# Kernel tuning notes

Hardware: AMD Instinct MI355X
Metric: run time of the kernel (lower is better)

## Reference

```python
import jax, jax.numpy as jnp
import numpy as np

KSIZE = 7       # patch size
STRIDE_Q = 4    # stride_1: query patch stride
STRIDE_KV = 1   # stride_2: key/value patch stride
SCALE = 10.0    # softmax_scale


def unfold(x, k, stride, pad):
    """torch.nn.Unfold equivalent. x:[B,C,H,W] -> [B, C*k*k, L] (c-major, then kh, kw)."""
    x = jnp.pad(x, ((0, 0), (0, 0), (pad, pad), (pad, pad)))
    B, C, Hp, Wp = x.shape
    nh = (Hp - k) // stride + 1
    nw = (Wp - k) // stride + 1
    sl = lambda i, n: slice(i, i + (n - 1) * stride + 1, stride)
    # [B, C, k*k, nh, nw]
    pat = jnp.stack([x[:, :, sl(i, nh), sl(j, nw)] for i in range(k) for j in range(k)], axis=2)
    return pat.reshape(B, C * k * k, nh * nw)


def fold(p, k, stride, pad, H, W):
    """torch.nn.functional.fold equivalent (overlap-add). p:[B, C*k*k, L] -> [B,C,H,W]."""
    B, D, L = p.shape
    C = D // (k * k)
    nh = (H + 2 * pad - k) // stride + 1
    nw = (W + 2 * pad - k) // stride + 1
    p = p.reshape(B, C, k, k, nh, nw)
    out = jnp.zeros((B, C, H + 2 * pad, W + 2 * pad), p.dtype)
    sl = lambda i, n: slice(i, i + (n - 1) * stride + 1, stride)
    for i in range(k):
        for j in range(k):
            out = out.at[:, :, sl(i, nh), sl(j, nw)].add(p[:, :, i, j])
    return out[:, :, pad:pad + H, pad:pad + W]


def conv1x1(x, w, bias):
    # w: [out, in]
    return jnp.einsum('bihw,oi->bohw', x, w) + bias[None, :, None, None]


def setup_inputs() -> dict:
    key = jax.random.key(0)
    ks = jax.random.split(key, 9)
    B, Cin, H, W = 4, 64, 128, 128
    Cit = 16
    s_in = 1.0 / np.sqrt(Cin)
    s_it = 1.0 / np.sqrt(Cit)
    return {
        'b': jax.random.normal(ks[0], (B, Cin, H, W), jnp.float32),
        'g_w': jax.random.normal(ks[1], (Cit, Cin), jnp.float32) * s_in,
        'g_b': jax.random.normal(ks[2], (Cit,), jnp.float32) * 0.01,
        'th_w': jax.random.normal(ks[3], (Cit, Cin), jnp.float32) * s_in,
        'th_b': jax.random.normal(ks[4], (Cit,), jnp.float32) * 0.01,
        'ph_w': jax.random.normal(ks[5], (Cit, Cin), jnp.float32) * s_in,
        'ph_b': jax.random.normal(ks[6], (Cit,), jnp.float32) * 0.01,
        'o_w': jax.random.normal(ks[7], (Cin, Cit), jnp.float32) * s_it,
        'o_b': jax.random.normal(ks[8], (Cin,), jnp.float32) * 0.01,
    }


def reference(b, g_w, g_b, th_w, th_b, ph_w, ph_b, o_w, o_b):
    B, Cin, H, W = b.shape
    pad = KSIZE // 2
    b1 = conv1x1(b, g_w, g_b)      # queries source  [B,16,H,W]
    b2 = conv1x1(b, th_w, th_b)    # values source
    b3 = conv1x1(b, ph_w, ph_b)    # keys source

    Q = unfold(b1, KSIZE, STRIDE_Q, pad).transpose(0, 2, 1)   # [B, L1, D]
    K = unfold(b3, KSIZE, STRIDE_KV, pad).transpose(0, 2, 1)  # [B, L2, D]
    V = unfold(b2, KSIZE, STRIDE_KV, pad).transpose(0, 2, 1)  # [B, L2, D]

    scores = jnp.einsum('bqd,bkd->bqk', Q, K)                 # [B, L1, L2]
    attn = jax.nn.softmax(scores * SCALE, axis=-1)
    Zp = jnp.einsum('bqk,bkd->bqd', attn, V).transpose(0, 2, 1)  # [B, D, L1]

    y = fold(Zp, KSIZE, STRIDE_Q, pad, H, W)                  # overlap-add
    Zc = fold(jnp.ones_like(Zp), KSIZE, STRIDE_Q, pad, H, W)  # overlap counts
    y = y / Zc
    y = conv1x1(y, o_w, o_b)
    return b + y
```

## Files before the change

### kernel.cpp

```cpp
#include <hip/hip_runtime.h>
#include <math.h>

#define NB 4
#define CIN 64
#define CIT 16
#define KS 7
#define PAD 3
#define HH 128
#define WW 128
#define HP 134
#define WPS 136
#define L1 1024
#define DD 784
#define SCALE_F 10.0f
#define WSCR 4.0f
#define TCAP 128

#define NPIX (HP * WPS)
#define NHWCF (NB * NPIX * CIT)
#define RSTR 2176

typedef __attribute__((ext_vector_type(4))) float f32x4;
typedef __attribute__((ext_vector_type(8))) short s16x8;
typedef __attribute__((ext_vector_type(4))) unsigned int u32x4;

__device__ __forceinline__ unsigned short f2bf(float f) {
    unsigned u = __float_as_uint(f);
    unsigned r = (u + 0x7FFFu + ((u >> 16) & 1u)) >> 16;
    return (unsigned short)r;
}

__global__ __launch_bounds__(256) void k_prep(
    const float* __restrict__ bin,
    const float* __restrict__ gw, const float* __restrict__ gb,
    const float* __restrict__ tw, const float* __restrict__ tb,
    const float* __restrict__ pw, const float* __restrict__ pb,
    float* __restrict__ b1f, float* __restrict__ b2f, float* __restrict__ b3f,
    unsigned short* __restrict__ b1n, unsigned short* __restrict__ b3n)
{
    int p = blockIdx.x * 256 + threadIdx.x;
    if (p >= NB * NPIX) return;
    int x = p % WPS; int r = p / WPS; int y = r % HP; int bb = r / HP;
    bool inter = (x >= PAD && x < PAD + WW && y >= PAD && y < PAD + HH);
    float v[CIN];
    if (inter) {
        int iy = y - PAD, ix = x - PAD;
        const float* src = bin + ((size_t)(bb * CIN) * HH + iy) * WW + ix;
        #pragma unroll
        for (int ci = 0; ci < CIN; ++ci) v[ci] = src[ci * HH * WW];
    }
    float a1v[CIT], a2v[CIT], a3v[CIT];
    unsigned short o1[CIT], o3[CIT];
    #pragma unroll
    for (int co = 0; co < CIT; ++co) {
        float a1 = 0.f, a2 = 0.f, a3 = 0.f;
        if (inter) {
            a1 = gb[co]; a2 = tb[co]; a3 = pb[co];
            #pragma unroll
            for (int ci = 0; ci < CIN; ++ci) {
                float vv = v[ci];
                a1 += gw[co * CIN + ci] * vv;
                a2 += tw[co * CIN + ci] * vv;
                a3 += pw[co * CIN + ci] * vv;
            }
        }
        a1v[co] = a1; a2v[co] = a2; a3v[co] = a3;
        o1[co] = f2bf(a1); o3[co] = f2bf(a3);
    }
    size_t pb16 = (size_t)p * CIT;
    #pragma unroll
    for (int g = 0; g < 4; ++g) {
        f32x4 w1 = {a1v[4*g], a1v[4*g+1], a1v[4*g+2], a1v[4*g+3]};
        f32x4 w2 = {a2v[4*g], a2v[4*g+1], a2v[4*g+2], a2v[4*g+3]};
        f32x4 w3 = {a3v[4*g], a3v[4*g+1], a3v[4*g+2], a3v[4*g+3]};
        *(f32x4*)(b1f + pb16 + 4*g) = w1;
        *(f32x4*)(b2f + pb16 + 4*g) = w2;
        *(f32x4*)(b3f + pb16 + 4*g) = w3;
    }
    unsigned pk1[8], pk3[8];
    #pragma unroll
    for (int kk = 0; kk < 8; ++kk) {
        pk1[kk] = (unsigned)o1[2 * kk] | ((unsigned)o1[2 * kk + 1] << 16);
        pk3[kk] = (unsigned)o3[2 * kk] | ((unsigned)o3[2 * kk + 1] << 16);
    }
    unsigned short* d1 = b1n + pb16;
    unsigned short* d3 = b3n + pb16;
    u32x4 w1a = {pk1[0], pk1[1], pk1[2], pk1[3]}, w1b = {pk1[4], pk1[5], pk1[6], pk1[7]};
    u32x4 w3a = {pk3[0], pk3[1], pk3[2], pk3[3]}, w3b = {pk3[4], pk3[5], pk3[6], pk3[7]};
    *(u32x4*)d1 = w1a; *(u32x4*)(d1 + 8) = w1b;
    *(u32x4*)d3 = w3a; *(u32x4*)(d3 + 8) = w3b;
}

__global__ __launch_bounds__(512, 2) void k_screen(
    const unsigned short* __restrict__ b1n, const unsigned short* __restrict__ b3n,
    _Float16* __restrict__ tmaxh)
{
    int blk = blockIdx.x;
    int qt = blk & 3;
    int qh = (blk >> 2) & 31;
    int bb = blk >> 7;
    int qstart_ky = qt * 32;
    int tid = threadIdx.x;
    int lane = tid & 63, w = tid >> 6;
    int lanelow = lane & 15;
    int h = (lane >> 5) & 1;
    int clo = (lane >> 4) & 1;

    __shared__ __align__(16) short smem[16 * RSTR];

    const unsigned short* b1nb = b1n + (size_t)bb * (NPIX * CIT);
    const unsigned short* b3nb = b3n + (size_t)bb * (NPIX * CIT);

    int qybase = 4 * qh;
    size_t qb0 = ((size_t)((bb * 64 + 2 * qh) * 16 + lanelow)) * 1024 + qt * 256 + w;
    size_t qb1 = ((size_t)((bb * 64 + 2 * qh + 1) * 16 + lanelow)) * 1024 + qt * 256 + w;

    for (int task = tid; task < 1600; task += 512) {
        int pp = task % 50, qq = task / 50;
        u32x4 lo = {0, 0, 0, 0}, hi = {0, 0, 0, 0};
        if (pp < 49) {
            int i = pp / 7, j = pp % 7;
            int qx = 4 * qq;
            const unsigned short* src = b1nb + ((size_t)(qybase + i) * WPS + qx + j) * CIT;
            lo = *(const u32x4*)src; hi = *(const u32x4*)(src + 8);
        }
        short* dst = smem + (qq * 50 + pp) * 16;
        *(u32x4*)dst = lo; *(u32x4*)(dst + 8) = hi;
    }
    __syncthreads();

    s16x8 B0[25], B1[25];
    #pragma unroll
    for (int s = 0; s < 25; ++s) {
        int ko = s * 32 + ((lane >> 4) & 3) * 8;
        B0[s] = *(const s16x8*)(smem + lanelow * 800 + ko);
        B1[s] = *(const s16x8*)(smem + (lanelow + 16) * 800 + ko);
    }
    __syncthreads();

    short* kring = smem;
    for (int task = tid; task < 16 * 272; task += 512) {
        int rr = task / 272, ch = task % 272;
        *(u32x4*)(kring + rr * RSTR + ch * 8) =
            *(const u32x4*)(b3nb + (size_t)(qstart_ky + rr) * (WPS * CIT) + ch * 8);
    }
    __syncthreads();

    int abase = (w * 16 + lanelow) * 16 + clo * 8;

    for (int p = 0; p < 4; ++p) {
        __builtin_amdgcn_s_setprio(1);
        for (int it8 = 0; it8 < 8; ++it8) {
            int it = 8 * p + it8;
            int ky = qstart_ky + it;
            f32x4 C0 = {0.f, 0.f, 0.f, 0.f}, C1 = {0.f, 0.f, 0.f, 0.f};
            #pragma unroll
            for (int s = 0; s < 25; ++s) {
                const int pe = 2 * s;
                const int po = (2 * s + 1 < 49) ? (2 * s + 1) : 0;
                const int ie = pe / 7, je = pe % 7;
                const int io = po / 7, jo = po % 7;
                int i_h = h ? io : ie;
                int j_h = h ? jo : je;
                int slot = (ky + i_h) & 15;
                const short* ap = kring + slot * RSTR + j_h * 16 + abase;
                s16x8 a0 = *(const s16x8*)ap;
                C0 = __builtin_amdgcn_mfma_f32_16x16x32_bf16(a0, B0[s], C0, 0, 0, 0);
                C1 = __builtin_amdgcn_mfma_f32_16x16x32_bf16(a0, B1[s], C1, 0, 0, 0);
            }
            float lm0 = fmaxf(fmaxf(C0[0], C0[1]), fmaxf(C0[2], C0[3]));
            lm0 = fmaxf(lm0, __shfl_xor(lm0, 16));
            lm0 = fmaxf(lm0, __shfl_xor(lm0, 32));
            float lm1 = fmaxf(fmaxf(C1[0], C1[1]), fmaxf(C1[2], C1[3]));
            lm1 = fmaxf(lm1, __shfl_xor(lm1, 16));
            lm1 = fmaxf(lm1, __shfl_xor(lm1, 32));
            if (lane < 16) {
                tmaxh[qb0 + it * 8] = (_Float16)lm0;
                tmaxh[qb1 + it * 8] = (_Float16)lm1;
            }
        }
        __builtin_amdgcn_s_setprio(0);
        __syncthreads();
        if (p < 3) {
            int rbase = qstart_ky + 8 * p + 16;
            for (int task = tid; task < 8 * 272; task += 512) {
                int rr = task / 272, ch = task % 272;
                int row = rbase + rr;
                int srow = (row < HP) ? row : (HP - 1);
                *(u32x4*)(kring + (row & 15) * RSTR + ch * 8) =
                    *(const u32x4*)(b3nb + (size_t)srow * (WPS * CIT) + ch * 8);
            }
            __syncthreads();
        }
    }
}

__global__ __launch_bounds__(256) void k_finalize(
    const float* __restrict__ b1f, const float* __restrict__ b2f,
    const float* __restrict__ b3f, const _Float16* __restrict__ tmaxh,
    float* __restrict__ Zp)
{
    int wv = threadIdx.x >> 6;
    int lane = threadIdx.x & 63;
    int gq = blockIdx.x * 4 + wv;
    int bb = gq >> 10, q = gq & 1023;
    int qh = q >> 5, qw = q & 31;
    int qy = qh * 4, qx = qw * 4;
    int ch = lane & 15, pbase = lane >> 4;

    __shared__ int tq[4][TCAP];

    const float* b1b = b1f + (size_t)bb * (NPIX * CIT);
    const float* b2b = b2f + (size_t)bb * (NPIX * CIT);
    const float* b3b = b3f + (size_t)bb * (NPIX * CIT);

    const _Float16* qb = tmaxh + ((size_t)((bb * 64 + (q >> 4)) * 16 + (q & 15))) * 1024;
    _Float16 tvh[16];
    *(u32x4*)&tvh[0] = *(const u32x4*)(qb + (size_t)lane * 16);
    *(u32x4*)&tvh[8] = *(const u32x4*)(qb + (size_t)lane * 16 + 8);
    float tv[16]; float mg = -1e30f;
    #pragma unroll
    for (int k = 0; k < 16; ++k) {
        tv[k] = (float)tvh[k];
        mg = fmaxf(mg, tv[k]);
    }
    #pragma unroll
    for (int o = 32; o > 0; o >>= 1) mg = fmaxf(mg, __shfl_xor(mg, o));
    float thr = mg - WSCR;

    int cnt = 0;
    #pragma unroll
    for (int k = 0; k < 16; ++k) {
        bool p = (tv[k] >= thr);
        unsigned long long mk = __ballot(p);
        if (p) {
            int pos = cnt + (int)__popcll(mk & ((1ull << lane) - 1ull));
            if (pos < TCAP) tq[wv][pos] = lane * 16 + k;
        }
        cnt += (int)__popcll(mk);
    }
    int nt = min(cnt, TCAP);
    int n = nt * 16;
    __syncthreads();

    float qreg[13]; int offs[13];
    int qorg = (qy * WPS + qx) * CIT;
    #pragma unroll
    for (int k = 0; k < 13; ++k) {
        int p = pbase + 4 * k;
        if (p < 49) {
            int pi = p / 7, pj = p % 7;
            offs[k] = (pi * WPS + pj) * CIT + ch;
            qreg[k] = b1b[qorg + offs[k]];
        } else { offs[k] = 0; qreg[k] = 0.f; }
    }

    float m = -1e30f, l = 0.f, acc[13];
    #pragma unroll
    for (int k = 0; k < 13; ++k) acc[k] = 0.f;

    for (int ci0 = 0; ci0 < n; ci0 += 4) {
        int kb[4];
        #pragma unroll
        for (int u = 0; u < 4; ++u) {
            int ci = ci0 + u;
            int e = tq[wv][ci >> 4];
            int ky = (e >> 8) * 32 + ((e >> 3) & 31);
            int kx = (e & 7) * 16 + (ci & 15);
            kb[u] = (ky * WPS + kx) * CIT;
        }
        float kv[4][13], vv[4][13];
        #pragma unroll
        for (int u = 0; u < 4; ++u) {
            #pragma unroll
            for (int k = 0; k < 13; ++k) {
                kv[u][k] = b3b[kb[u] + offs[k]];
                vv[u][k] = b2b[kb[u] + offs[k]];
            }
        }
        float s[4];
        #pragma unroll
        for (int u = 0; u < 4; ++u) {
            float t = 0.f;
            #pragma unroll
            for (int k = 0; k < 13; ++k) t += qreg[k] * kv[u][k];
            #pragma unroll
            for (int o = 32; o > 0; o >>= 1) t += __shfl_xor(t, o);
            s[u] = t;
        }
        float mnew = fmaxf(m, fmaxf(fmaxf(s[0], s[1]), fmaxf(s[2], s[3])));
        float sc = __expf(SCALE_F * (m - mnew));
        float w0 = __expf(SCALE_F * (s[0] - mnew));
        float w1 = __expf(SCALE_F * (s[1] - mnew));
        float w2 = __expf(SCALE_F * (s[2] - mnew));
        float w3 = __expf(SCALE_F * (s[3] - mnew));
        l = l * sc + (w0 + w1 + w2 + w3);
        #pragma unroll
        for (int k = 0; k < 13; ++k)
            acc[k] = acc[k] * sc + w0 * vv[0][k] + w1 * vv[1][k]
                                 + w2 * vv[2][k] + w3 * vv[3][k];
        m = mnew;
    }

    float inv = (n > 0) ? (1.f / l) : 0.f;
    float* zq = Zp + (size_t)gq * DD;
    #pragma unroll
    for (int k = 0; k < 13; ++k) {
        int d = lane + 64 * k;
        if (d < DD) zq[d] = acc[k] * inv;
    }
}

__global__ __launch_bounds__(256) void k_fold(
    const float* __restrict__ bin, const float* __restrict__ ow,
    const float* __restrict__ ob, const float* __restrict__ Zp,
    float* __restrict__ outp)
{
    int p = blockIdx.x * 256 + threadIdx.x;
    if (p >= NB * HH * WW) return;
    int ox = p % WW; int r = p / WW; int oy = r % HH; int bb = r / HH;
    int yp = oy + PAD, xp = ox + PAD;
    int qh0 = (yp - 3) >> 2, qh1 = min(31, yp >> 2);
    int qw0 = (xp - 3) >> 2, qw1 = min(31, xp >> 2);
    float cnt = (float)((qh1 - qh0 + 1) * (qw1 - qw0 + 1));
    float y16[CIT];
    #pragma unroll
    for (int c = 0; c < CIT; ++c) y16[c] = 0.f;
    for (int qhh = qh0; qhh <= qh1; ++qhh) {
        int i = yp - 4 * qhh;
        for (int qww = qw0; qww <= qw1; ++qww) {
            int j = xp - 4 * qww;
            const float* zb = Zp + (size_t)((bb << 10) + qhh * 32 + qww) * DD + (i * 7 + j) * CIT;
            #pragma unroll
            for (int c = 0; c < CIT; ++c) y16[c] += zb[c];
        }
    }
    float icnt = 1.f / cnt;
    #pragma unroll
    for (int c = 0; c < CIT; ++c) y16[c] *= icnt;
    size_t oidx = ((size_t)(bb * CIN) * HH + oy) * WW + ox;
    for (int co = 0; co < CIN; ++co) {
        float a = ob[co];
        #pragma unroll
        for (int c = 0; c < CIT; ++c) a += ow[co * CIT + c] * y16[c];
        outp[oidx + (size_t)co * HH * WW] = bin[oidx + (size_t)co * HH * WW] + a;
    }
}

extern "C" void kernel_launch(void* const* d_in, const int* in_sizes, int n_in,
                              void* d_out, int out_size, void* d_ws, size_t ws_size,
                              hipStream_t stream) {
    (void)in_sizes; (void)n_in; (void)out_size; (void)ws_size;
    const float* bin = (const float*)d_in[0];
    const float* gw  = (const float*)d_in[1];
    const float* gb  = (const float*)d_in[2];
    const float* tw  = (const float*)d_in[3];
    const float* tb  = (const float*)d_in[4];
    const float* pw  = (const float*)d_in[5];
    const float* pb  = (const float*)d_in[6];
    const float* ow  = (const float*)d_in[7];
    const float* ob  = (const float*)d_in[8];

    float* outp = (float*)d_out;
    float* b3f = outp;
    float* b1f = outp + NHWCF;
    unsigned short* b3n = (unsigned short*)(outp + 2 * (size_t)NHWCF);
    unsigned short* b1n = b3n + NHWCF;

    float* ws = (float*)d_ws;
    float* b2f = ws;
    float* Zp  = ws + NHWCF;
    _Float16* tmaxh = (_Float16*)(ws + NHWCF + (size_t)NB * L1 * DD);

    hipLaunchKernelGGL(k_prep, dim3((NB * NPIX + 255) / 256), dim3(256), 0, stream,
                       bin, gw, gb, tw, tb, pw, pb, b1f, b2f, b3f, b1n, b3n);
    hipLaunchKernelGGL(k_screen, dim3(512), dim3(512), 0, stream,
                       b1n, b3n, tmaxh);
    hipLaunchKernelGGL(k_finalize, dim3(1024), dim3(256), 0, stream,
                       b1f, b2f, b3f, tmaxh, Zp);
    hipLaunchKernelGGL(k_fold, dim3((NB * HH * WW + 255) / 256), dim3(256), 0, stream,
                       bin, ow, ob, Zp, outp);
}
```

Measured before the change: 230.8 us.

## Split screening kernel into 16-row tiles and tighten the candidate threshold

The screening kernel now gives each block 16 key rows instead of 32. The grid doubles to 1024 blocks, and the ring-buffer refill loop with its extra barriers is replaced by a single 22-row LDS load. LDS offsets are precomputed per MFMA step and the row loop is fully unrolled, which cuts address arithmetic. The finalize kernel's tile index decode is updated to match the new tmax layout. The screening margin WSCR drops from 4.0 to 3.5, so fewer tiles are recomputed exactly, at some risk of dropping tiles that matter to the softmax.

```diff
diff --git a/kernel.cpp b/kernel.cpp
--- a/kernel.cpp
+++ b/kernel.cpp
@@ -13,12 +13,13 @@
 #define L1 1024
 #define DD 784
 #define SCALE_F 10.0f
-#define WSCR 4.0f
+#define WSCR 3.5f
 #define TCAP 128
 
 #define NPIX (HP * WPS)
 #define NHWCF (NB * NPIX * CIT)
 #define RSTR 2176
+#define NROWS 22
 
 typedef __attribute__((ext_vector_type(4))) float f32x4;
 typedef __attribute__((ext_vector_type(8))) short s16x8;
@@ -96,24 +97,24 @@
     _Float16* __restrict__ tmaxh)
 {
     int blk = blockIdx.x;
-    int qt = blk & 3;
-    int qh = (blk >> 2) & 31;
-    int bb = blk >> 7;
-    int qstart_ky = qt * 32;
+    int qth = blk & 7;
+    int qh = (blk >> 3) & 31;
+    int bb = blk >> 8;
+    int ky0 = qth * 16;
     int tid = threadIdx.x;
     int lane = tid & 63, w = tid >> 6;
     int lanelow = lane & 15;
     int h = (lane >> 5) & 1;
     int clo = (lane >> 4) & 1;
 
-    __shared__ __align__(16) short smem[16 * RSTR];
+    __shared__ __align__(16) short smem[NROWS * RSTR];
 
     const unsigned short* b1nb = b1n + (size_t)bb * (NPIX * CIT);
     const unsigned short* b3nb = b3n + (size_t)bb * (NPIX * CIT);
 
     int qybase = 4 * qh;
-    size_t qb0 = ((size_t)((bb * 64 + 2 * qh) * 16 + lanelow)) * 1024 + qt * 256 + w;
-    size_t qb1 = ((size_t)((bb * 64 + 2 * qh + 1) * 16 + lanelow)) * 1024 + qt * 256 + w;
+    size_t qb0 = ((size_t)((bb * 64 + 2 * qh) * 16 + lanelow)) * 1024 + w;
+    size_t qb1 = ((size_t)((bb * 64 + 2 * qh + 1) * 16 + lanelow)) * 1024 + w;
 
     for (int task = tid; task < 1600; task += 512) {
         int pp = task % 50, qq = task / 50;
@@ -138,61 +139,49 @@
     }
     __syncthreads();
 
-    short* kring = smem;
-    for (int task = tid; task < 16 * 272; task += 512) {
+    for (int task = tid; task < NROWS * 272; task += 512) {
         int rr = task / 272, ch = task % 272;
-        *(u32x4*)(kring + rr * RSTR + ch * 8) =
-            *(const u32x4*)(b3nb + (size_t)(qstart_ky + rr) * (WPS * CIT) + ch * 8);
+        *(u32x4*)(smem + rr * RSTR + ch * 8) =
+            *(const u32x4*)(b3nb + (size_t)(ky0 + rr) * (WPS * CIT) + ch * 8);
     }
     __syncthreads();
 
     int abase = (w * 16 + lanelow) * 16 + clo * 8;
-
-    for (int p = 0; p < 4; ++p) {
-        __builtin_amdgcn_s_setprio(1);
-        for (int it8 = 0; it8 < 8; ++it8) {
-            int it = 8 * p + it8;
-            int ky = qstart_ky + it;
-            f32x4 C0 = {0.f, 0.f, 0.f, 0.f}, C1 = {0.f, 0.f, 0.f, 0.f};
-            #pragma unroll
-            for (int s = 0; s < 25; ++s) {
-                const int pe = 2 * s;
-                const int po = (2 * s + 1 < 49) ? (2 * s + 1) : 0;
-                const int ie = pe / 7, je = pe % 7;
-                const int io = po / 7, jo = po % 7;
-                int i_h = h ? io : ie;
-                int j_h = h ? jo : je;
-                int slot = (ky + i_h) & 15;
-                const short* ap = kring + slot * RSTR + j_h * 16 + abase;
-                s16x8 a0 = *(const s16x8*)ap;
-                C0 = __builtin_amdgcn_mfma_f32_16x16x32_bf16(a0, B0[s], C0, 0, 0, 0);
-                C1 = __builtin_amdgcn_mfma_f32_16x16x32_bf16(a0, B1[s], C1, 0, 0, 0);
-            }
-            float lm0 = fmaxf(fmaxf(C0[0], C0[1]), fmaxf(C0[2], C0[3]));
-            lm0 = fmaxf(lm0, __shfl_xor(lm0, 16));
-            lm0 = fmaxf(lm0, __shfl_xor(lm0, 32));
-            float lm1 = fmaxf(fmaxf(C1[0], C1[1]), fmaxf(C1[2], C1[3]));
-            lm1 = fmaxf(lm1, __shfl_xor(lm1, 16));
-            lm1 = fmaxf(lm1, __shfl_xor(lm1, 32));
-            if (lane < 16) {
-                tmaxh[qb0 + it * 8] = (_Float16)lm0;
-                tmaxh[qb1 + it * 8] = (_Float16)lm1;
-            }
-        }
-        __builtin_amdgcn_s_setprio(0);
-        __syncthreads();
-        if (p < 3) {
-            int rbase = qstart_ky + 8 * p + 16;
-            for (int task = tid; task < 8 * 272; task += 512) {
-                int rr = task / 272, ch = task % 272;
-                int row = rbase + rr;
-                int srow = (row < HP) ? row : (HP - 1);
-                *(u32x4*)(kring + (row & 15) * RSTR + ch * 8) =
-                    *(const u32x4*)(b3nb + (size_t)srow * (WPS * CIT) + ch * 8);
-            }
-            __syncthreads();
-        }
-    }
+    int voff[25];
+    #pragma unroll
+    for (int s = 0; s < 25; ++s) {
+        const int pe = 2 * s;
+        const int po = (2 * s + 1 < 49) ? (2 * s + 1) : 0;
+        const int ie = pe / 7, je = pe % 7;
+        const int io = po / 7, jo = po % 7;
+        const int offE = (ie * RSTR + je * 16) * 2;
+        const int offO = (io * RSTR + jo * 16) * 2;
+        voff[s] = abase * 2 + (h ? offO : offE);
+    }
+    const char* kb = (const char*)smem;
+
+    __builtin_amdgcn_s_setprio(1);
+    #pragma unroll
+    for (int it = 0; it < 16; ++it) {
+        f32x4 C0 = {0.f, 0.f, 0.f, 0.f}, C1 = {0.f, 0.f, 0.f, 0.f};
+        #pragma unroll
+        for (int s = 0; s < 25; ++s) {
+            s16x8 a0 = *(const s16x8*)(kb + voff[s] + it * 4352);
+            C0 = __builtin_amdgcn_mfma_f32_16x16x32_bf16(a0, B0[s], C0, 0, 0, 0);
+            C1 = __builtin_amdgcn_mfma_f32_16x16x32_bf16(a0, B1[s], C1, 0, 0, 0);
+        }
+        float lm0 = fmaxf(fmaxf(C0[0], C0[1]), fmaxf(C0[2], C0[3]));
+        lm0 = fmaxf(lm0, __shfl_xor(lm0, 16));
+        lm0 = fmaxf(lm0, __shfl_xor(lm0, 32));
+        float lm1 = fmaxf(fmaxf(C1[0], C1[1]), fmaxf(C1[2], C1[3]));
+        lm1 = fmaxf(lm1, __shfl_xor(lm1, 16));
+        lm1 = fmaxf(lm1, __shfl_xor(lm1, 32));
+        if (lane < 16) {
+            tmaxh[qb0 + (size_t)(ky0 + it) * 8] = (_Float16)lm0;
+            tmaxh[qb1 + (size_t)(ky0 + it) * 8] = (_Float16)lm1;
+        }
+    }
+    __builtin_amdgcn_s_setprio(0);
 }
 
 __global__ __launch_bounds__(256) void k_finalize(
@@ -265,7 +254,7 @@
         for (int u = 0; u < 4; ++u) {
             int ci = ci0 + u;
             int e = tq[wv][ci >> 4];
-            int ky = (e >> 8) * 32 + ((e >> 3) & 31);
+            int ky = e >> 3;
             int kx = (e & 7) * 16 + (ci & 15);
             kb[u] = (ky * WPS + kx) * CIT;
         }
@@ -374,7 +363,7 @@
 
     hipLaunchKernelGGL(k_prep, dim3((NB * NPIX + 255) / 256), dim3(256), 0, stream,
                        bin, gw, gb, tw, tb, pw, pb, b1f, b2f, b3f, b1n, b3n);
-    hipLaunchKernelGGL(k_screen, dim3(512), dim3(512), 0, stream,
+    hipLaunchKernelGGL(k_screen, dim3(1024), dim3(512), 0, stream,
                        b1n, b3n, tmaxh);
     hipLaunchKernelGGL(k_finalize, dim3(1024), dim3(256), 0, stream,
                        b1f, b2f, b3f, tmaxh, Zp);
```

Measured after the change: 239.4 us. +3.7%, slower.
